# Performance work log

Measured on AMD Instinct MI355X. Metric: run time of the kernel, lower is better.

## Reference

```python
import jax, jax.numpy as jnp
import numpy as np

B = 65536      # batch
S = 256        # state_dim
A = 8          # n_agents
NA = 16        # n_actions
K = 10         # num_kernel
H = 64         # adv_hypernet_embed
AD = A * NA    # action_dim
D = S + AD     # state_dim + action_dim


def setup_inputs() -> dict:
    key = jax.random.key(0)
    ks = jax.random.split(key, 20)
    sc = 0.05
    inp = {
        'states': jax.random.normal(ks[0], (B, S), jnp.float32),
        'actions_onehot': jax.random.uniform(ks[1], (B, A, NA), jnp.float32),
        # key extractors: S -> H -> H -> 1, stacked over K kernels
        'kW1': jax.random.normal(ks[2], (K, H, S), jnp.float32) * sc,
        'kb1': jnp.zeros((K, H), jnp.float32),
        'kW2': jax.random.normal(ks[3], (K, H, H), jnp.float32) * sc,
        'kb2': jnp.zeros((K, H), jnp.float32),
        'kW3': jax.random.normal(ks[4], (K, 1, H), jnp.float32) * sc,
        'kb3': jnp.zeros((K, 1), jnp.float32),
        # agents extractors: S -> H -> H -> A
        'aW1': jax.random.normal(ks[5], (K, H, S), jnp.float32) * sc,
        'ab1': jnp.zeros((K, H), jnp.float32),
        'aW2': jax.random.normal(ks[6], (K, H, H), jnp.float32) * sc,
        'ab2': jnp.zeros((K, H), jnp.float32),
        'aW3': jax.random.normal(ks[7], (K, A, H), jnp.float32) * sc,
        'ab3': jnp.zeros((K, A), jnp.float32),
        # action extractors: S+AD -> H -> H -> A
        'cW1': jax.random.normal(ks[8], (K, H, D), jnp.float32) * sc,
        'cb1': jnp.zeros((K, H), jnp.float32),
        'cW2': jax.random.normal(ks[9], (K, H, H), jnp.float32) * sc,
        'cb2': jnp.zeros((K, H), jnp.float32),
        'cW3': jax.random.normal(ks[10], (K, A, H), jnp.float32) * sc,
        'cb3': jnp.zeros((K, A), jnp.float32),
    }
    return inp


def _mlp3(x, W1, b1, W2, b2, W3, b3):
    # x: [B, in] ; W1: [K, H, in] -> batched over K kernels in one GEMM
    h = jax.nn.relu(jnp.einsum('bd,khd->bkh', x, W1) + b1)        # [B,K,H]
    h = jax.nn.relu(jnp.einsum('bkh,kgh->bkg', h, W2) + b2)       # [B,K,H]
    return jnp.einsum('bkh,koh->bko', h, W3) + b3                 # [B,K,out]


def reference(states, actions_onehot,
              kW1, kb1, kW2, kb2, kW3, kb3,
              aW1, ab1, aW2, ab2, aW3, ab3,
              cW1, cb1, cW2, cb2, cW3, cb3):
    actions_flat = actions_onehot.reshape(states.shape[0], -1)    # [B, A*NA]
    data = jnp.concatenate([states, actions_flat], axis=1)        # [B, S+AD]

    x_key = jnp.abs(_mlp3(states, kW1, kb1, kW2, kb2, kW3, kb3)) + 1e-10   # [B,K,1]
    x_agents = jax.nn.sigmoid(_mlp3(states, aW1, ab1, aW2, ab2, aW3, ab3)) # [B,K,A]
    x_action = jax.nn.sigmoid(_mlp3(data, cW1, cb1, cW2, cb2, cW3, cb3))   # [B,K,A]

    # broadcast key over agents, multiply gates, sum over the K kernels
    head_attend = jnp.sum(x_key * x_agents * x_action, axis=1)    # [B,A]
    return head_attend
```

## Files before the change

kernel.cpp:

```cpp
#include <hip/hip_runtime.h>
#include <hip/hip_bf16.h>

#define Bsz 65536
#define Sdim 256
#define Aag 8
#define Kk 10
#define ADdim 128

#define SLAB_K_ELEMS 72704
#define NET_ELEMS 21504

typedef float f32x4 __attribute__((ext_vector_type(4)));
typedef __bf16 bf16x8 __attribute__((ext_vector_type(8)));

#define MFMA(a, b, cacc) __builtin_amdgcn_mfma_f32_16x16x32_bf16((a), (b), (cacc), 0, 0, 0)

__device__ __forceinline__ __bf16 f2bf(float f) {
    unsigned int u = __float_as_uint(f);
    unsigned int r = (u + 0x7fffu + ((u >> 16) & 1u)) >> 16;
    union { unsigned short s; __bf16 b; } cv;
    cv.s = (unsigned short)r;
    return cv.b;
}

__device__ __forceinline__ unsigned int pack_bf2(float a, float b) {
    union { unsigned short s[2]; unsigned int u; } cv;
    union { unsigned short s; __bf16 b; } x;
    x.b = f2bf(a); cv.s[0] = x.s;
    x.b = f2bf(b); cv.s[1] = x.s;
    return cv.u;
}

__device__ __forceinline__ bf16x8 cvt8(float4 lo, float4 hi) {
    bf16x8 v;
    v[0] = f2bf(lo.x); v[1] = f2bf(lo.y); v[2] = f2bf(lo.z); v[3] = f2bf(lo.w);
    v[4] = f2bf(hi.x); v[5] = f2bf(hi.y); v[6] = f2bf(hi.z); v[7] = f2bf(hi.w);
    return v;
}

__device__ __forceinline__ int gperm(int n) {
    return ((n >> 5) << 5) + (((n >> 2) & 3) << 3) + (((n >> 4) & 1) << 2) + (n & 3);
}

__global__ void prep_weights(const float* __restrict__ kW1, const float* __restrict__ aW1,
                             const float* __restrict__ cW1, const float* __restrict__ kW2,
                             const float* __restrict__ aW2, const float* __restrict__ cW2,
                             const float* __restrict__ kW3, const float* __restrict__ aW3,
                             const float* __restrict__ cW3, __bf16* __restrict__ out) {
    int gid = blockIdx.x * 256 + threadIdx.x;
    if (gid >= 90880) return;
    int k = gid / 9088;
    int r = gid - k * 9088;
    int t, cn;
    if (r < 2688)      { t = 0; cn = r; }
    else if (r < 5376) { t = 1; cn = r - 2688; }
    else               { t = 2; cn = r - 5376; }
    const int KN = (t == 2) ? 384 : 256;
    const int CPR = KN / 8;
    const float* W1 = (t == 0) ? kW1 : (t == 1) ? aW1 : cW1;
    const float* W2 = (t == 0) ? kW2 : (t == 1) ? aW2 : cW2;
    const float* W3 = (t == 0) ? kW3 : (t == 1) ? aW3 : cW3;
    const int rows3 = (t == 0) ? 1 : 8;
    int dstchunk;
    const float* src = nullptr;
    if (cn < 64 * CPR) {
        int n = cn / CPR, k8 = cn - n * CPR;
        src = W1 + ((size_t)(k * 64 + gperm(n))) * KN + k8 * 8;
        dstchunk = n * CPR + (k8 ^ (n & 7));
    } else if (cn < 64 * CPR + 512) {
        int c2 = cn - 64 * CPR;
        int n = c2 >> 3, k8 = c2 & 7;
        src = W2 + ((size_t)(k * 64 + gperm(n))) * 64 + k8 * 8;
        dstchunk = 64 * CPR + n * 8 + (k8 ^ (n & 7));
    } else {
        int c3 = cn - 64 * CPR - 512;
        int n = c3 >> 3, k8 = c3 & 7;
        if (n < rows3) src = W3 + ((size_t)(k * rows3 + n)) * 64 + k8 * 8;
        dstchunk = 64 * CPR + 512 + n * 8 + (k8 ^ (n & 7));
    }
    bf16x8 v;
#pragma unroll
    for (int e = 0; e < 8; ++e) v[e] = src ? f2bf(src[e]) : (__bf16)0.0f;
    *(bf16x8*)(out + (size_t)k * SLAB_K_ELEMS + t * NET_ELEMS + dstchunk * 8) = v;
}

__device__ __forceinline__ void stage(const __bf16* __restrict__ src, __bf16* dst,
                                      int nchunks, int wave, int lane) {
    const char* g = (const char*)src + lane * 16;
    for (int ci = wave; ci < nchunks; ci += 8) {
        __builtin_amdgcn_global_load_lds(
            (const __attribute__((address_space(1))) void*)(g + ci * 1024),
            (__attribute__((address_space(3))) void*)((char*)dst + ci * 1024), 16, 0, 0);
    }
}

__device__ __forceinline__ bf16x8 frag_from_hp(const unsigned int (&hp)[4][2], int kb) {
    int4 u = {(int)hp[kb * 2][0], (int)hp[kb * 2][1], (int)hp[kb * 2 + 1][0], (int)hp[kb * 2 + 1][1]};
    return __builtin_bit_cast(bf16x8, u);
}

template <int KB, int MODE>
__device__ __forceinline__ void compute_net(
    const __bf16* __restrict__ W, const bf16x8 (&xf)[2][8],
    const float* __restrict__ actions, int rowbase,
    int q, int c, int k,
    const float* __restrict__ b1p, const float* __restrict__ b2p, const float* __restrict__ b3p,
    float (&keyv)[2], float (&ag)[2][4], float (&outacc)[2][4]) {
    constexpr int CPR = KB * 4;
    constexpr int W2O = 64 * CPR * 8;
    constexpr int W3O = W2O + 4096;

    bf16x8 xa[2][4];
    if (MODE == 2) {
#pragma unroll
        for (int s = 0; s < 2; ++s) {
            const float* ap = actions + (size_t)(rowbase + s * 16 + c) * ADdim + q * 8;
#pragma unroll
            for (int kb = 0; kb < 4; ++kb)
                xa[s][kb] = cvt8(*(const float4*)(ap + kb * 32), *(const float4*)(ap + kb * 32 + 4));
        }
    }

    f32x4 acc[4][2];
#pragma unroll
    for (int mt = 0; mt < 4; ++mt) {
        int base = ((mt >> 1) << 5) + (q << 3) + ((mt & 1) << 2);
        float4 bv = *(const float4*)(b1p + k * 64 + base);
        f32x4 b = {bv.x, bv.y, bv.z, bv.w};
        acc[mt][0] = b; acc[mt][1] = b;
    }
#pragma unroll
    for (int kb = 0; kb < KB; ++kb) {
        bf16x8 b0 = (kb < 8) ? xf[0][kb] : xa[0][kb - 8];
        bf16x8 b1 = (kb < 8) ? xf[1][kb] : xa[1][kb - 8];
#pragma unroll
        for (int mt = 0; mt < 4; ++mt) {
            int n = mt * 16 + c;
            bf16x8 a = *(const bf16x8*)(W + ((n * CPR + ((kb * 4 + q) ^ (n & 7))) << 3));
            acc[mt][0] = MFMA(a, b0, acc[mt][0]);
            acc[mt][1] = MFMA(a, b1, acc[mt][1]);
        }
    }
    unsigned int hp[2][4][2];
#pragma unroll
    for (int s = 0; s < 2; ++s)
#pragma unroll
        for (int mt = 0; mt < 4; ++mt) {
            hp[s][mt][0] = pack_bf2(fmaxf(acc[mt][s][0], 0.f), fmaxf(acc[mt][s][1], 0.f));
            hp[s][mt][1] = pack_bf2(fmaxf(acc[mt][s][2], 0.f), fmaxf(acc[mt][s][3], 0.f));
        }

    f32x4 acc2[4][2];
#pragma unroll
    for (int mt = 0; mt < 4; ++mt) {
        int base = ((mt >> 1) << 5) + (q << 3) + ((mt & 1) << 2);
        float4 bv = *(const float4*)(b2p + k * 64 + base);
        f32x4 b = {bv.x, bv.y, bv.z, bv.w};
        acc2[mt][0] = b; acc2[mt][1] = b;
    }
#pragma unroll
    for (int kb = 0; kb < 2; ++kb) {
        bf16x8 bh0 = frag_from_hp(hp[0], kb);
        bf16x8 bh1 = frag_from_hp(hp[1], kb);
#pragma unroll
        for (int mt = 0; mt < 4; ++mt) {
            int n = mt * 16 + c;
            bf16x8 a2 = *(const bf16x8*)(W + W2O + ((n * 8 + ((kb * 4 + q) ^ (n & 7))) << 3));
            acc2[mt][0] = MFMA(a2, bh0, acc2[mt][0]);
            acc2[mt][1] = MFMA(a2, bh1, acc2[mt][1]);
        }
    }
#pragma unroll
    for (int s = 0; s < 2; ++s)
#pragma unroll
        for (int mt = 0; mt < 4; ++mt) {
            hp[s][mt][0] = pack_bf2(fmaxf(acc2[mt][s][0], 0.f), fmaxf(acc2[mt][s][1], 0.f));
            hp[s][mt][1] = pack_bf2(fmaxf(acc2[mt][s][2], 0.f), fmaxf(acc2[mt][s][3], 0.f));
        }

    f32x4 acc3[2];
    if (MODE == 0) {
        float b3 = b3p[k];
        f32x4 z = {0.f, 0.f, 0.f, 0.f};
        if (q == 0) z[0] = b3;
        acc3[0] = z; acc3[1] = z;
    } else {
        f32x4 z = {0.f, 0.f, 0.f, 0.f};
        if (q < 2) {
            float4 bv = *(const float4*)(b3p + k * 8 + q * 4);
            z = {bv.x, bv.y, bv.z, bv.w};
        }
        acc3[0] = z; acc3[1] = z;
    }
#pragma unroll
    for (int kb = 0; kb < 2; ++kb) {
        bf16x8 a3 = *(const bf16x8*)(W + W3O + ((c * 8 + ((kb * 4 + q) ^ (c & 7))) << 3));
#pragma unroll
        for (int s = 0; s < 2; ++s) acc3[s] = MFMA(a3, frag_from_hp(hp[s], kb), acc3[s]);
    }
#pragma unroll
    for (int s = 0; s < 2; ++s) {
        if (MODE == 0) {
            float v = __shfl(acc3[s][0], c, 64);
            keyv[s] = fabsf(v) + 1e-10f;
        } else if (MODE == 1) {
#pragma unroll
            for (int i = 0; i < 4; ++i) ag[s][i] = 1.f / (1.f + __expf(-acc3[s][i]));
        } else {
#pragma unroll
            for (int i = 0; i < 4; ++i)
                outacc[s][i] += keyv[s] * ag[s][i] * (1.f / (1.f + __expf(-acc3[s][i])));
        }
    }
}

__global__ __launch_bounds__(512, 2) void qplex_main(
    const float* __restrict__ states, const float* __restrict__ actions,
    const __bf16* __restrict__ wbf,
    const float* __restrict__ b1k, const float* __restrict__ b2k, const float* __restrict__ b3k,
    const float* __restrict__ b1a, const float* __restrict__ b2a, const float* __restrict__ b3a,
    const float* __restrict__ b1c, const float* __restrict__ b2c, const float* __restrict__ b3c,
    float* __restrict__ out) {
    __shared__ __bf16 WB[2][29696];

    const int tid = threadIdx.x;
    const int lane = tid & 63;
    const int wave = tid >> 6;
    const int q = lane >> 4;
    const int c = lane & 15;
    const int rowbase = blockIdx.x * 256 + wave * 32;

    stage(wbf, WB[0], 42, wave, lane);

    bf16x8 xf[2][8];
#pragma unroll
    for (int s = 0; s < 2; ++s) {
        const float* srow = states + (size_t)(rowbase + s * 16 + c) * Sdim + q * 8;
#pragma unroll
        for (int kb = 0; kb < 8; ++kb)
            xf[s][kb] = cvt8(*(const float4*)(srow + kb * 32), *(const float4*)(srow + kb * 32 + 4));
    }

    float keyv[2];
    float ag[2][4];
    float outacc[2][4];
#pragma unroll
    for (int s = 0; s < 2; ++s) {
        keyv[s] = 0.f;
#pragma unroll
        for (int i = 0; i < 4; ++i) { ag[s][i] = 0.f; outacc[s][i] = 0.f; }
    }

    __syncthreads();

    for (int k = 0; k < Kk; ++k) {
        const __bf16* kslab = wbf + (size_t)k * SLAB_K_ELEMS;
        stage(kslab + NET_ELEMS, WB[(k + 1) & 1], 42, wave, lane);
        compute_net<8, 0>(&WB[k & 1][0], xf, actions, rowbase, q, c, k,
                          b1k, b2k, b3k, keyv, ag, outacc);
        __syncthreads();
        stage(kslab + 2 * NET_ELEMS, WB[k & 1], 58, wave, lane);
        compute_net<8, 1>(&WB[(k + 1) & 1][0], xf, actions, rowbase, q, c, k,
                          b1a, b2a, b3a, keyv, ag, outacc);
        __syncthreads();
        if (k < Kk - 1) stage(kslab + SLAB_K_ELEMS, WB[(k + 1) & 1], 42, wave, lane);
        compute_net<12, 2>(&WB[k & 1][0], xf, actions, rowbase, q, c, k,
                           b1c, b2c, b3c, keyv, ag, outacc);
        __syncthreads();
    }

    if (q < 2) {
#pragma unroll
        for (int s = 0; s < 2; ++s) {
            int r = rowbase + s * 16 + c;
            float4 v = {outacc[s][0], outacc[s][1], outacc[s][2], outacc[s][3]};
            *(float4*)(out + (size_t)r * Aag + q * 4) = v;
        }
    }
}

extern "C" void kernel_launch(void* const* d_in, const int* in_sizes, int n_in,
                              void* d_out, int out_size, void* d_ws, size_t ws_size,
                              hipStream_t stream) {
    const float* states = (const float*)d_in[0];
    const float* actions = (const float*)d_in[1];
    const float* kW1 = (const float*)d_in[2];
    const float* kb1 = (const float*)d_in[3];
    const float* kW2 = (const float*)d_in[4];
    const float* kb2 = (const float*)d_in[5];
    const float* kW3 = (const float*)d_in[6];
    const float* kb3 = (const float*)d_in[7];
    const float* aW1 = (const float*)d_in[8];
    const float* ab1 = (const float*)d_in[9];
    const float* aW2 = (const float*)d_in[10];
    const float* ab2 = (const float*)d_in[11];
    const float* aW3 = (const float*)d_in[12];
    const float* ab3 = (const float*)d_in[13];
    const float* cW1 = (const float*)d_in[14];
    const float* cb1 = (const float*)d_in[15];
    const float* cW2 = (const float*)d_in[16];
    const float* cb2 = (const float*)d_in[17];
    const float* cW3 = (const float*)d_in[18];
    const float* cb3 = (const float*)d_in[19];
    float* out = (float*)d_out;
    __bf16* wbf = (__bf16*)d_ws;

    prep_weights<<<355, 256, 0, stream>>>(kW1, aW1, cW1, kW2, aW2, cW2, kW3, aW3, cW3, wbf);
    qplex_main<<<256, 512, 0, stream>>>(states, actions, wbf, kb1, kb2, kb3,
                                        ab1, ab2, ab3, cb1, cb2, cb3, out);
}
```

Measured before the change: 294.3 us.

## Shrink blocks, single-buffer weight LDS, and cut per-thread register live ranges

Blocks shrink from 512 to 256 threads, each covering 128 rows, so the grid grows from 256 to 512 blocks. The weight slab in LDS is now single-buffered with a sync before and after each stage, which drops the double-buffer overlap between loading and compute. Inside compute_net each output tile is accumulated and packed immediately, action fragments are loaded inline instead of held, and agent gates are stored as packed fp16. Together these aim to lower register and LDS pressure so more waves fit per CU, at the cost of exposed weight-load latency and fp16 rounding of the gates.

```diff
diff --git a/kernel.cpp b/kernel.cpp
--- a/kernel.cpp
+++ b/kernel.cpp
@@ -1,5 +1,6 @@
 #include <hip/hip_runtime.h>
 #include <hip/hip_bf16.h>
+#include <hip/hip_fp16.h>
 
 #define Bsz 65536
 #define Sdim 256
@@ -29,6 +30,19 @@
     x.b = f2bf(a); cv.s[0] = x.s;
     x.b = f2bf(b); cv.s[1] = x.s;
     return cv.u;
+}
+
+__device__ __forceinline__ unsigned int packh2(float a, float b) {
+    union { __half h[2]; unsigned int u; } v;
+    v.h[0] = __float2half(a);
+    v.h[1] = __float2half(b);
+    return v.u;
+}
+
+__device__ __forceinline__ float unpackh(unsigned int w, int i) {
+    union { unsigned int u; __half h[2]; } v;
+    v.u = w;
+    return __half2float(v.h[i]);
 }
 
 __device__ __forceinline__ bf16x8 cvt8(float4 lo, float4 hi) {
@@ -87,7 +101,7 @@
 __device__ __forceinline__ void stage(const __bf16* __restrict__ src, __bf16* dst,
                                       int nchunks, int wave, int lane) {
     const char* g = (const char*)src + lane * 16;
-    for (int ci = wave; ci < nchunks; ci += 8) {
+    for (int ci = wave; ci < nchunks; ci += 4) {
         __builtin_amdgcn_global_load_lds(
             (const __attribute__((address_space(1))) void*)(g + ci * 1024),
             (__attribute__((address_space(3))) void*)((char*)dst + ci * 1024), 16, 0, 0);
@@ -102,81 +116,65 @@
 template <int KB, int MODE>
 __device__ __forceinline__ void compute_net(
     const __bf16* __restrict__ W, const bf16x8 (&xf)[2][8],
-    const float* __restrict__ actions, int rowbase,
-    int q, int c, int k,
+    const float* __restrict__ actions, int rowbase, int q, int c, int k,
     const float* __restrict__ b1p, const float* __restrict__ b2p, const float* __restrict__ b3p,
-    float (&keyv)[2], float (&ag)[2][4], float (&outacc)[2][4]) {
+    float (&keyv)[2], unsigned int (&ag)[2][2], float (&outacc)[2][4]) {
     constexpr int CPR = KB * 4;
     constexpr int W2O = 64 * CPR * 8;
     constexpr int W3O = W2O + 4096;
 
-    bf16x8 xa[2][4];
-    if (MODE == 2) {
-#pragma unroll
-        for (int s = 0; s < 2; ++s) {
-            const float* ap = actions + (size_t)(rowbase + s * 16 + c) * ADdim + q * 8;
-#pragma unroll
-            for (int kb = 0; kb < 4; ++kb)
-                xa[s][kb] = cvt8(*(const float4*)(ap + kb * 32), *(const float4*)(ap + kb * 32 + 4));
-        }
-    }
-
-    f32x4 acc[4][2];
+    unsigned int hpA[2][4][2];
 #pragma unroll
     for (int mt = 0; mt < 4; ++mt) {
-        int base = ((mt >> 1) << 5) + (q << 3) + ((mt & 1) << 2);
+        const int n = mt * 16 + c;
+        const int base = ((mt >> 1) << 5) + (q << 3) + ((mt & 1) << 2);
         float4 bv = *(const float4*)(b1p + k * 64 + base);
-        f32x4 b = {bv.x, bv.y, bv.z, bv.w};
-        acc[mt][0] = b; acc[mt][1] = b;
-    }
-#pragma unroll
-    for (int kb = 0; kb < KB; ++kb) {
-        bf16x8 b0 = (kb < 8) ? xf[0][kb] : xa[0][kb - 8];
-        bf16x8 b1 = (kb < 8) ? xf[1][kb] : xa[1][kb - 8];
-#pragma unroll
-        for (int mt = 0; mt < 4; ++mt) {
-            int n = mt * 16 + c;
+        f32x4 acc0 = {bv.x, bv.y, bv.z, bv.w};
+        f32x4 acc1 = acc0;
+#pragma unroll
+        for (int kb = 0; kb < 8; ++kb) {
             bf16x8 a = *(const bf16x8*)(W + ((n * CPR + ((kb * 4 + q) ^ (n & 7))) << 3));
-            acc[mt][0] = MFMA(a, b0, acc[mt][0]);
-            acc[mt][1] = MFMA(a, b1, acc[mt][1]);
-        }
-    }
-    unsigned int hp[2][4][2];
-#pragma unroll
-    for (int s = 0; s < 2; ++s)
-#pragma unroll
-        for (int mt = 0; mt < 4; ++mt) {
-            hp[s][mt][0] = pack_bf2(fmaxf(acc[mt][s][0], 0.f), fmaxf(acc[mt][s][1], 0.f));
-            hp[s][mt][1] = pack_bf2(fmaxf(acc[mt][s][2], 0.f), fmaxf(acc[mt][s][3], 0.f));
-        }
-
-    f32x4 acc2[4][2];
+            acc0 = MFMA(a, xf[0][kb], acc0);
+            acc1 = MFMA(a, xf[1][kb], acc1);
+        }
+        if (MODE == 2) {
+            const float* ap0 = actions + (size_t)(rowbase + c) * ADdim + q * 8;
+#pragma unroll
+            for (int kb = 8; kb < 12; ++kb) {
+                bf16x8 a = *(const bf16x8*)(W + ((n * CPR + ((kb * 4 + q) ^ (n & 7))) << 3));
+                const float* p0 = ap0 + (kb - 8) * 32;
+                const float* p1 = p0 + 16 * ADdim;
+                bf16x8 b0 = cvt8(*(const float4*)p0, *(const float4*)(p0 + 4));
+                bf16x8 b1 = cvt8(*(const float4*)p1, *(const float4*)(p1 + 4));
+                acc0 = MFMA(a, b0, acc0);
+                acc1 = MFMA(a, b1, acc1);
+            }
+        }
+        hpA[0][mt][0] = pack_bf2(fmaxf(acc0[0], 0.f), fmaxf(acc0[1], 0.f));
+        hpA[0][mt][1] = pack_bf2(fmaxf(acc0[2], 0.f), fmaxf(acc0[3], 0.f));
+        hpA[1][mt][0] = pack_bf2(fmaxf(acc1[0], 0.f), fmaxf(acc1[1], 0.f));
+        hpA[1][mt][1] = pack_bf2(fmaxf(acc1[2], 0.f), fmaxf(acc1[3], 0.f));
+    }
+
+    unsigned int hpB[2][4][2];
 #pragma unroll
     for (int mt = 0; mt < 4; ++mt) {
-        int base = ((mt >> 1) << 5) + (q << 3) + ((mt & 1) << 2);
+        const int n = mt * 16 + c;
+        const int base = ((mt >> 1) << 5) + (q << 3) + ((mt & 1) << 2);
         float4 bv = *(const float4*)(b2p + k * 64 + base);
-        f32x4 b = {bv.x, bv.y, bv.z, bv.w};
-        acc2[mt][0] = b; acc2[mt][1] = b;
-    }
-#pragma unroll
-    for (int kb = 0; kb < 2; ++kb) {
-        bf16x8 bh0 = frag_from_hp(hp[0], kb);
-        bf16x8 bh1 = frag_from_hp(hp[1], kb);
-#pragma unroll
-        for (int mt = 0; mt < 4; ++mt) {
-            int n = mt * 16 + c;
+        f32x4 acc0 = {bv.x, bv.y, bv.z, bv.w};
+        f32x4 acc1 = acc0;
+#pragma unroll
+        for (int kb = 0; kb < 2; ++kb) {
             bf16x8 a2 = *(const bf16x8*)(W + W2O + ((n * 8 + ((kb * 4 + q) ^ (n & 7))) << 3));
-            acc2[mt][0] = MFMA(a2, bh0, acc2[mt][0]);
-            acc2[mt][1] = MFMA(a2, bh1, acc2[mt][1]);
-        }
-    }
-#pragma unroll
-    for (int s = 0; s < 2; ++s)
-#pragma unroll
-        for (int mt = 0; mt < 4; ++mt) {
-            hp[s][mt][0] = pack_bf2(fmaxf(acc2[mt][s][0], 0.f), fmaxf(acc2[mt][s][1], 0.f));
-            hp[s][mt][1] = pack_bf2(fmaxf(acc2[mt][s][2], 0.f), fmaxf(acc2[mt][s][3], 0.f));
-        }
+            acc0 = MFMA(a2, frag_from_hp(hpA[0], kb), acc0);
+            acc1 = MFMA(a2, frag_from_hp(hpA[1], kb), acc1);
+        }
+        hpB[0][mt][0] = pack_bf2(fmaxf(acc0[0], 0.f), fmaxf(acc0[1], 0.f));
+        hpB[0][mt][1] = pack_bf2(fmaxf(acc0[2], 0.f), fmaxf(acc0[3], 0.f));
+        hpB[1][mt][0] = pack_bf2(fmaxf(acc1[0], 0.f), fmaxf(acc1[1], 0.f));
+        hpB[1][mt][1] = pack_bf2(fmaxf(acc1[2], 0.f), fmaxf(acc1[3], 0.f));
+    }
 
     f32x4 acc3[2];
     if (MODE == 0) {
@@ -196,7 +194,7 @@
     for (int kb = 0; kb < 2; ++kb) {
         bf16x8 a3 = *(const bf16x8*)(W + W3O + ((c * 8 + ((kb * 4 + q) ^ (c & 7))) << 3));
 #pragma unroll
-        for (int s = 0; s < 2; ++s) acc3[s] = MFMA(a3, frag_from_hp(hp[s], kb), acc3[s]);
+        for (int s = 0; s < 2; ++s) acc3[s] = MFMA(a3, frag_from_hp(hpB[s], kb), acc3[s]);
     }
 #pragma unroll
     for (int s = 0; s < 2; ++s) {
@@ -204,33 +202,37 @@
             float v = __shfl(acc3[s][0], c, 64);
             keyv[s] = fabsf(v) + 1e-10f;
         } else if (MODE == 1) {
-#pragma unroll
-            for (int i = 0; i < 4; ++i) ag[s][i] = 1.f / (1.f + __expf(-acc3[s][i]));
+            float s0 = 1.f / (1.f + __expf(-acc3[s][0]));
+            float s1 = 1.f / (1.f + __expf(-acc3[s][1]));
+            float s2 = 1.f / (1.f + __expf(-acc3[s][2]));
+            float s3 = 1.f / (1.f + __expf(-acc3[s][3]));
+            ag[s][0] = packh2(s0, s1);
+            ag[s][1] = packh2(s2, s3);
         } else {
 #pragma unroll
-            for (int i = 0; i < 4; ++i)
-                outacc[s][i] += keyv[s] * ag[s][i] * (1.f / (1.f + __expf(-acc3[s][i])));
-        }
-    }
-}
-
-__global__ __launch_bounds__(512, 2) void qplex_main(
+            for (int i = 0; i < 4; ++i) {
+                float agf = unpackh(ag[s][i >> 1], i & 1);
+                outacc[s][i] += keyv[s] * agf * (1.f / (1.f + __expf(-acc3[s][i])));
+            }
+        }
+    }
+}
+
+__global__ __launch_bounds__(256, 2) void qplex_main(
     const float* __restrict__ states, const float* __restrict__ actions,
     const __bf16* __restrict__ wbf,
     const float* __restrict__ b1k, const float* __restrict__ b2k, const float* __restrict__ b3k,
     const float* __restrict__ b1a, const float* __restrict__ b2a, const float* __restrict__ b3a,
     const float* __restrict__ b1c, const float* __restrict__ b2c, const float* __restrict__ b3c,
     float* __restrict__ out) {
-    __shared__ __bf16 WB[2][29696];
+    __shared__ __bf16 WB[29696];
 
     const int tid = threadIdx.x;
     const int lane = tid & 63;
     const int wave = tid >> 6;
     const int q = lane >> 4;
     const int c = lane & 15;
-    const int rowbase = blockIdx.x * 256 + wave * 32;
-
-    stage(wbf, WB[0], 42, wave, lane);
+    const int rowbase = blockIdx.x * 128 + wave * 32;
 
     bf16x8 xf[2][8];
 #pragma unroll
@@ -242,31 +244,30 @@
     }
 
     float keyv[2];
-    float ag[2][4];
+    unsigned int ag[2][2];
     float outacc[2][4];
 #pragma unroll
     for (int s = 0; s < 2; ++s) {
         keyv[s] = 0.f;
-#pragma unroll
-        for (int i = 0; i < 4; ++i) { ag[s][i] = 0.f; outacc[s][i] = 0.f; }
-    }
-
-    __syncthreads();
+        ag[s][0] = 0u; ag[s][1] = 0u;
+#pragma unroll
+        for (int i = 0; i < 4; ++i) outacc[s][i] = 0.f;
+    }
 
     for (int k = 0; k < Kk; ++k) {
         const __bf16* kslab = wbf + (size_t)k * SLAB_K_ELEMS;
-        stage(kslab + NET_ELEMS, WB[(k + 1) & 1], 42, wave, lane);
-        compute_net<8, 0>(&WB[k & 1][0], xf, actions, rowbase, q, c, k,
-                          b1k, b2k, b3k, keyv, ag, outacc);
-        __syncthreads();
-        stage(kslab + 2 * NET_ELEMS, WB[k & 1], 58, wave, lane);
-        compute_net<8, 1>(&WB[(k + 1) & 1][0], xf, actions, rowbase, q, c, k,
-                          b1a, b2a, b3a, keyv, ag, outacc);
-        __syncthreads();
-        if (k < Kk - 1) stage(kslab + SLAB_K_ELEMS, WB[(k + 1) & 1], 42, wave, lane);
-        compute_net<12, 2>(&WB[k & 1][0], xf, actions, rowbase, q, c, k,
-                           b1c, b2c, b3c, keyv, ag, outacc);
-        __syncthreads();
+        __syncthreads();
+        stage(kslab, WB, 42, wave, lane);
+        __syncthreads();
+        compute_net<8, 0>(WB, xf, actions, rowbase, q, c, k, b1k, b2k, b3k, keyv, ag, outacc);
+        __syncthreads();
+        stage(kslab + NET_ELEMS, WB, 42, wave, lane);
+        __syncthreads();
+        compute_net<8, 1>(WB, xf, actions, rowbase, q, c, k, b1a, b2a, b3a, keyv, ag, outacc);
+        __syncthreads();
+        stage(kslab + 2 * NET_ELEMS, WB, 58, wave, lane);
+        __syncthreads();
+        compute_net<12, 2>(WB, xf, actions, rowbase, q, c, k, b1c, b2c, b3c, keyv, ag, outacc);
     }
 
     if (q < 2) {
@@ -306,6 +307,6 @@
     __bf16* wbf = (__bf16*)d_ws;
 
     prep_weights<<<355, 256, 0, stream>>>(kW1, aW1, cW1, kW2, aW2, cW2, kW3, aW3, cW3, wbf);
-    qplex_main<<<256, 512, 0, stream>>>(states, actions, wbf, kb1, kb2, kb3,
-                                        ab1, ab2, ab3, cb1, cb2, cb3, out);
-}
+    qplex_main<<<Bsz / 128, 256, 0, stream>>>(states, actions, wbf, kb1, kb2, kb3,
+                                              ab1, ab2, ab3, cb1, cb2, cb3, out);
+}
```

Result: slower. 322.9 us (+9.7%).
